# Kernel optimization log

Hardware: AMD Instinct MI355X
Metric: run time of the kernel (lower is better)

The kernel has to match this reference:

```python
import jax, jax.numpy as jnp
import numpy as np

HEADS = 8
DIM_HEAD = 64
DIM = 256
INNER = HEADS * DIM_HEAD  # 512


def setup_inputs() -> dict:
    key = jax.random.key(0)
    ks = jax.random.split(key, 5)
    b_times_r, n = 32, 1024
    x = jax.random.normal(ks[0], (b_times_r, n, DIM), dtype=jnp.float32)
    # nn.Linear weights stored as (in, out) so y = x @ W
    Wq = jax.random.normal(ks[1], (DIM, INNER), dtype=jnp.float32) * 0.02
    Wkv = jax.random.normal(ks[2], (DIM, 2 * INNER), dtype=jnp.float32) * 0.02
    Wout = jax.random.normal(ks[3], (INNER, DIM), dtype=jnp.float32) * 0.02
    bout = jax.random.normal(ks[4], (DIM,), dtype=jnp.float32) * 0.02
    return {"x": x, "Wq": Wq, "Wkv": Wkv, "Wout": Wout, "bout": bout, "tie_attn_dim": 32}


def reference(x, Wq, Wkv, Wout, bout, tie_attn_dim):
    r = tie_attn_dim
    br, n, _ = x.shape
    b = br // r
    q = x @ Wq                                   # (b*r, n, inner)
    k, v = jnp.split(x @ Wkv, 2, axis=-1)        # (b*r, n, inner) each

    def split_heads(t):
        # (b*r) n (h d) -> b r h n d
        return t.reshape(b, r, n, HEADS, DIM_HEAD).transpose(0, 1, 3, 2, 4)

    q, k, v = map(split_heads, (q, k, v))
    scale = (DIM_HEAD ** -0.5) * (r ** -0.5)
    # tied attention: sum logits over the MSA row dim r
    dots = jnp.einsum('brhid,brhjd->bhij', q, k) * scale  # (b, h, n, n)
    attn = jax.nn.softmax(dots, axis=-1)
    out = jnp.einsum('bhij,brhjd->brhid', attn, v)        # (b, r, h, n, d)
    out = out.transpose(0, 1, 3, 2, 4).reshape(br, n, INNER)
    return out @ Wout + bout
```

## Files before the change

kernel.cpp:

```cpp
#include <hip/hip_runtime.h>
#include <math.h>

typedef unsigned short bf16u;
typedef __attribute__((ext_vector_type(8))) short short8;
typedef __attribute__((ext_vector_type(4))) float f32x4;

__device__ __forceinline__ bf16u f2bf(float f) {
    unsigned int u = __float_as_uint(f);
    u += 0x7fffu + ((u >> 16) & 1u);
    return (bf16u)(u >> 16);
}
__device__ __forceinline__ float bf2f(bf16u h) {
    return __uint_as_float(((unsigned int)h) << 16);
}

__device__ __forceinline__ void gload16(const void* g, void* s) {
    __builtin_amdgcn_global_load_lds((const __attribute__((address_space(1))) void*)g,
                                     (__attribute__((address_space(3))) void*)s, 16, 0, 0);
}

#define MM(a_, b_, c_) c_ = __builtin_amdgcn_mfma_f32_16x16x32_bf16(a_, b_, c_, 0, 0, 0)
#define BAR() __builtin_amdgcn_s_barrier()

#define STG() do { if (q < nht) { \
    const int t_ = q >> 2, p_ = q & 3; \
    const bf16u* P_ = (p_ < 2) ? B : A; \
    const long s_ = ((p_ < 2) ? brow : arow) + ((p_ & 1) ? r128 : 0) + t_ * 64; \
    bf16u* d_ = S + ((t_ & 1) << 15) + ((p_ < 2) ? 16384 : 0) + ((p_ & 1) << 12) + (w << 9); \
    gload16(P_ + s_, d_); \
    gload16(P_ + s_ + 32, d_ + 8192); \
  } ++q; } while (0)

#define RDA(dst, t, m, kk) dst = *(const short8*)(S + (((t) & 1) << 15) + ((kk) << 13) + ((wr * 8 + (m)) << 9) + (l << 3))
#define RDB(dst, t, n, kk) dst = *(const short8*)(S + (((t) & 1) << 15) + 16384 + ((kk) << 13) + ((wc * 4 + (n)) << 9) + (l << 3))

#define KTILE(t, VMASM) do { \
   \
  RDA(af[0][0],t,0,0); RDA(af[0][1],t,0,1); RDA(af[1][0],t,1,0); RDA(af[1][1],t,1,1); \
  RDA(af[2][0],t,2,0); RDA(af[2][1],t,2,1); RDA(af[3][0],t,3,0); RDA(af[3][1],t,3,1); \
  RDB(b0[0][0],t,0,0); RDB(b0[0][1],t,0,1); RDB(b0[1][0],t,1,0); RDB(b0[1][1],t,1,1); \
  STG(); \
  BAR(); \
  __builtin_amdgcn_s_setprio(1); \
  MM(af[0][0],b0[0][0],acc[0][0]); MM(af[0][1],b0[0][1],acc[0][0]); \
  MM(af[0][0],b0[1][0],acc[0][1]); MM(af[0][1],b0[1][1],acc[0][1]); \
  MM(af[1][0],b0[0][0],acc[1][0]); MM(af[1][1],b0[0][1],acc[1][0]); \
  MM(af[1][0],b0[1][0],acc[1][1]); MM(af[1][1],b0[1][1],acc[1][1]); \
  MM(af[2][0],b0[0][0],acc[2][0]); MM(af[2][1],b0[0][1],acc[2][0]); \
  MM(af[2][0],b0[1][0],acc[2][1]); MM(af[2][1],b0[1][1],acc[2][1]); \
  MM(af[3][0],b0[0][0],acc[3][0]); MM(af[3][1],b0[0][1],acc[3][0]); \
  MM(af[3][0],b0[1][0],acc[3][1]); MM(af[3][1],b0[1][1],acc[3][1]); \
  __builtin_amdgcn_s_setprio(0); \
  BAR(); \
   \
  RDB(b1[0][0],t,2,0); RDB(b1[0][1],t,2,1); RDB(b1[1][0],t,3,0); RDB(b1[1][1],t,3,1); \
  STG(); \
  BAR(); \
  __builtin_amdgcn_s_setprio(1); \
  MM(af[0][0],b1[0][0],acc[0][2]); MM(af[0][1],b1[0][1],acc[0][2]); \
  MM(af[0][0],b1[1][0],acc[0][3]); MM(af[0][1],b1[1][1],acc[0][3]); \
  MM(af[1][0],b1[0][0],acc[1][2]); MM(af[1][1],b1[0][1],acc[1][2]); \
  MM(af[1][0],b1[1][0],acc[1][3]); MM(af[1][1],b1[1][1],acc[1][3]); \
  MM(af[2][0],b1[0][0],acc[2][2]); MM(af[2][1],b1[0][1],acc[2][2]); \
  MM(af[2][0],b1[1][0],acc[2][3]); MM(af[2][1],b1[1][1],acc[2][3]); \
  MM(af[3][0],b1[0][0],acc[3][2]); MM(af[3][1],b1[0][1],acc[3][2]); \
  MM(af[3][0],b1[1][0],acc[3][3]); MM(af[3][1],b1[1][1],acc[3][3]); \
  __builtin_amdgcn_s_setprio(0); \
  BAR(); \
   \
  RDA(af[0][0],t,4,0); RDA(af[0][1],t,4,1); RDA(af[1][0],t,5,0); RDA(af[1][1],t,5,1); \
  RDA(af[2][0],t,6,0); RDA(af[2][1],t,6,1); RDA(af[3][0],t,7,0); RDA(af[3][1],t,7,1); \
  STG(); \
  BAR(); \
  __builtin_amdgcn_s_setprio(1); \
  MM(af[0][0],b1[0][0],acc[4][2]); MM(af[0][1],b1[0][1],acc[4][2]); \
  MM(af[0][0],b1[1][0],acc[4][3]); MM(af[0][1],b1[1][1],acc[4][3]); \
  MM(af[1][0],b1[0][0],acc[5][2]); MM(af[1][1],b1[0][1],acc[5][2]); \
  MM(af[1][0],b1[1][0],acc[5][3]); MM(af[1][1],b1[1][1],acc[5][3]); \
  MM(af[2][0],b1[0][0],acc[6][2]); MM(af[2][1],b1[0][1],acc[6][2]); \
  MM(af[2][0],b1[1][0],acc[6][3]); MM(af[2][1],b1[1][1],acc[6][3]); \
  MM(af[3][0],b1[0][0],acc[7][2]); MM(af[3][1],b1[0][1],acc[7][2]); \
  MM(af[3][0],b1[1][0],acc[7][3]); MM(af[3][1],b1[1][1],acc[7][3]); \
  __builtin_amdgcn_s_setprio(0); \
  BAR(); \
   \
  STG(); \
  BAR(); \
  __builtin_amdgcn_s_setprio(1); \
  MM(af[0][0],b0[0][0],acc[4][0]); MM(af[0][1],b0[0][1],acc[4][0]); \
  MM(af[0][0],b0[1][0],acc[4][1]); MM(af[0][1],b0[1][1],acc[4][1]); \
  MM(af[1][0],b0[0][0],acc[5][0]); MM(af[1][1],b0[0][1],acc[5][0]); \
  MM(af[1][0],b0[1][0],acc[5][1]); MM(af[1][1],b0[1][1],acc[5][1]); \
  MM(af[2][0],b0[0][0],acc[6][0]); MM(af[2][1],b0[0][1],acc[6][0]); \
  MM(af[2][0],b0[1][0],acc[6][1]); MM(af[2][1],b0[1][1],acc[6][1]); \
  MM(af[3][0],b0[0][0],acc[7][0]); MM(af[3][1],b0[0][1],acc[7][0]); \
  MM(af[3][0],b0[1][0],acc[7][1]); MM(af[3][1],b0[1][1],acc[7][1]); \
  __builtin_amdgcn_s_setprio(0); \
  VMASM; \
  BAR(); \
} while (0)

template<int EPI>
__global__ __launch_bounds__(512, 2) void gemm8(
    const bf16u* __restrict__ Aall, const bf16u* __restrict__ Ball, int K,
    long sAz, long sBz,
    bf16u* __restrict__ D0, bf16u* __restrict__ D1, bf16u* __restrict__ D2,
    float* __restrict__ Df, const float* __restrict__ bias, float scale)
{
    const int gx = gridDim.x, gy = gridDim.y;
    const int nwg = gx * gy * gridDim.z;
    int flat = blockIdx.x + gx * (blockIdx.y + gy * blockIdx.z);
    int swz = (nwg & 7) ? flat : (flat & 7) * (nwg >> 3) + (flat >> 3);
    const int bx = swz % gx;
    int tq = swz / gx;
    const int by = tq % gy;
    const int z = tq / gy;

    const int tid = threadIdx.x;
    const int l = tid & 63, w = tid >> 6;
    const int fr = l & 15, fq = l >> 4;
    const int wr = w >> 2, wc = w & 3;
    const bf16u* A = Aall + (long)z * sAz;
    const bf16u* B = Ball + (long)z * sBz;
    const int m0 = by << 8, n0 = bx << 8;

    __shared__ __align__(16) bf16u S[65536];

    f32x4 acc[8][4];
#pragma unroll
    for (int i = 0; i < 8; ++i)
#pragma unroll
        for (int j = 0; j < 4; ++j) acc[i][j] = (f32x4){0.f, 0.f, 0.f, 0.f};

    const int NT = K >> 6;
    const int nht = NT << 2;
    const int NI = NT >> 1;
    int q = 0;

    const long arow = (long)(m0 + w * 16 + fr) * K + fq * 8;
    const long brow = (long)(n0 + w * 16 + fr) * K + fq * 8;
    const long r128 = (long)128 * K;

    STG(); STG(); STG(); STG(); STG(); STG();
    asm volatile("s_waitcnt vmcnt(4)" ::: "memory");
    BAR();

    short8 af[4][2], b0[2][2], b1[2][2];

    for (int i = 0; i < NI - 1; ++i) {
        KTILE(2 * i,     asm volatile("s_waitcnt vmcnt(4)" ::: "memory"));
        KTILE(2 * i + 1, asm volatile("s_waitcnt vmcnt(4)" ::: "memory"));
    }
    KTILE(2 * NI - 2, asm volatile("s_waitcnt vmcnt(0)" ::: "memory"));
    KTILE(2 * NI - 1, (void)0);

    const int colb = n0 + wc * 64;
    const int rowb = m0 + wr * 128;
    if constexpr (EPI == 1) {
        if (n0 >= 1024) {
            __syncthreads();
#pragma unroll
            for (int m = 0; m < 8; ++m)
#pragma unroll
                for (int n = 0; n < 4; ++n) {
                    const int cl = wc * 64 + n * 16 + fr;
                    const int rl = wr * 128 + m * 16 + fq * 4;
                    ushort4 pk;
                    pk.x = f2bf(acc[m][n][0]); pk.y = f2bf(acc[m][n][1]);
                    pk.z = f2bf(acc[m][n][2]); pk.w = f2bf(acc[m][n][3]);
                    *(ushort4*)(S + cl * 256 + rl) = pk;
                }
            __syncthreads();
            const int c2 = n0 - 1024;
            const int rr = m0 >> 10, i0 = m0 & 1023;
            const int rowt = tid >> 5;
            const int c0 = (tid & 31) * 8;
#pragma unroll
            for (int p = 0; p < 16; ++p) {
                const int row = p * 16 + rowt;
                const int hd = c2 + row;
                const int h = hd >> 6, d = hd & 63;
                *(short8*)(D2 + (((long)(h * 2048 + rr * 64 + d)) << 10) + i0 + c0)
                    = *(const short8*)(S + row * 256 + c0);
            }
        } else {
#pragma unroll
            for (int m = 0; m < 8; ++m)
#pragma unroll
                for (int n = 0; n < 4; ++n) {
                    const int col = colb + n * 16 + fr;
                    const int rb = rowb + m * 16 + fq * 4;
#pragma unroll
                    for (int r = 0; r < 4; ++r) {
                        const int row = rb + r;
                        const int rr = row >> 10, i = row & 1023;
                        const float val = acc[m][n][r];
                        if (col < 512) {
                            const int h = col >> 6, d = col & 63;
                            D0[((long)(h * 1024 + i) << 11) + rr * 64 + d] = f2bf(val);
                        } else {
                            const int c = col - 512, h = c >> 6, d = c & 63;
                            D1[((long)(h * 1024 + i) << 11) + rr * 64 + d] = f2bf(val);
                        }
                    }
                }
        }
    } else if constexpr (EPI == 2) {
#pragma unroll
        for (int m = 0; m < 8; ++m)
#pragma unroll
            for (int n = 0; n < 4; ++n) {
                const int col = colb + n * 16 + fr;
                const int rb = rowb + m * 16 + fq * 4;
#pragma unroll
                for (int r = 0; r < 4; ++r)
                    D0[((long)z << 20) + ((long)(rb + r) << 10) + col] = f2bf(acc[m][n][r] * scale);
            }
    } else if constexpr (EPI == 3) {
#pragma unroll
        for (int m = 0; m < 8; ++m)
#pragma unroll
            for (int n = 0; n < 4; ++n) {
                const int col = colb + n * 16 + fr;
                const int cb = col >> 6, d = col & 63;
                const int rb = rowb + m * 16 + fq * 4;
#pragma unroll
                for (int r = 0; r < 4; ++r)
                    D0[((long)(cb * 1024 + rb + r) << 9) + z * 64 + d] = f2bf(acc[m][n][r]);
            }
    } else {
#pragma unroll
        for (int m = 0; m < 8; ++m)
#pragma unroll
            for (int n = 0; n < 4; ++n) {
                const int col = colb + n * 16 + fr;
                const int rb = rowb + m * 16 + fq * 4;
#pragma unroll
                for (int r = 0; r < 4; ++r)
                    Df[(long)(rb + r) * 256 + col] = acc[m][n][r] + bias[col];
            }
    }
}

__global__ __launch_bounds__(256) void cvt_x(const float* __restrict__ in,
                                             bf16u* __restrict__ out) {
    const long idx = (long)(blockIdx.x * 256 + threadIdx.x) * 4;
    const float4 v = *(const float4*)(in + idx);
    ushort4 o;
    o.x = f2bf(v.x); o.y = f2bf(v.y); o.z = f2bf(v.z); o.w = f2bf(v.w);
    *(ushort4*)(out + idx) = o;
}

__global__ __launch_bounds__(256) void transpose_cvt(const float* __restrict__ in,
                                                     bf16u* __restrict__ out,
                                                     int R, int C) {
    const int idx = blockIdx.x * 256 + threadIdx.x;
    if (idx < R * C) {
        const int r = idx / C, c = idx % C;
        out[(long)c * R + r] = f2bf(in[idx]);
    }
}

__global__ __launch_bounds__(256) void softmax_rows(bf16u* __restrict__ att) {
    const long base = (long)blockIdx.x << 10;
    const int tid = threadIdx.x;
    const uint2 u = *(const uint2*)(att + base + tid * 4);
    const float v0 = bf2f(u.x & 0xffffu), v1 = bf2f(u.x >> 16);
    const float v2 = bf2f(u.y & 0xffffu), v3 = bf2f(u.y >> 16);
    float m = fmaxf(fmaxf(v0, v1), fmaxf(v2, v3));
#pragma unroll
    for (int o = 32; o; o >>= 1) m = fmaxf(m, __shfl_xor(m, o));
    __shared__ float red[8];
    if ((tid & 63) == 0) red[tid >> 6] = m;
    __syncthreads();
    m = fmaxf(fmaxf(red[0], red[1]), fmaxf(red[2], red[3]));
    const float e0 = __expf(v0 - m), e1 = __expf(v1 - m);
    const float e2 = __expf(v2 - m), e3 = __expf(v3 - m);
    float s = e0 + e1 + e2 + e3;
#pragma unroll
    for (int o = 32; o; o >>= 1) s += __shfl_xor(s, o);
    if ((tid & 63) == 0) red[4 + (tid >> 6)] = s;
    __syncthreads();
    const float inv = 1.0f / (red[4] + red[5] + red[6] + red[7]);
    uint2 o2;
    o2.x = (unsigned)f2bf(e0 * inv) | ((unsigned)f2bf(e1 * inv) << 16);
    o2.y = (unsigned)f2bf(e2 * inv) | ((unsigned)f2bf(e3 * inv) << 16);
    *(uint2*)(att + base + tid * 4) = o2;
}

extern "C" void kernel_launch(void* const* d_in, const int* in_sizes, int n_in,
                              void* d_out, int out_size, void* d_ws, size_t ws_size,
                              hipStream_t stream) {
    (void)in_sizes; (void)n_in; (void)out_size; (void)ws_size;
    const float* x    = (const float*)d_in[0];
    const float* Wq   = (const float*)d_in[1];
    const float* Wkv  = (const float*)d_in[2];
    const float* Wout = (const float*)d_in[3];
    const float* bout = (const float*)d_in[4];
    float* out = (float*)d_out;

    char* ws = (char*)d_ws;
    bf16u* xb    = (bf16u*)(ws);
    bf16u* WqkvT = (bf16u*)(ws + 16777216);
    bf16u* WoutT = (bf16u*)(ws + 17563648);
    bf16u* Qt    = (bf16u*)(ws + 17825792);
    bf16u* Kt    = (bf16u*)(ws + 51380224);
    bf16u* Vt2   = (bf16u*)(ws + 84934656);
    bf16u* att   = (bf16u*)(ws + 118489088);
    bf16u* out2  = (bf16u*)(ws + 135266304);

    cvt_x<<<8192, 256, 0, stream>>>(x, xb);
    transpose_cvt<<<512, 256, 0, stream>>>(Wq, WqkvT, 256, 512);
    transpose_cvt<<<1024, 256, 0, stream>>>(Wkv, WqkvT + 512 * 256, 256, 1024);
    transpose_cvt<<<512, 256, 0, stream>>>(Wout, WoutT, 512, 256);

    const float scale = 1.0f / (8.0f * sqrtf(32.0f));

    gemm8<1><<<dim3(6, 128, 1), 512, 0, stream>>>(
        xb, WqkvT, 256, 0, 0, Qt, Kt, Vt2, nullptr, nullptr, 0.f);

    gemm8<2><<<dim3(4, 4, 8), 512, 0, stream>>>(
        Qt, Kt, 2048, 1024L * 2048, 1024L * 2048, att, nullptr, nullptr, nullptr, nullptr, scale);

    softmax_rows<<<8192, 256, 0, stream>>>(att);

    gemm8<3><<<dim3(8, 4, 8), 512, 0, stream>>>(
        att, Vt2, 1024, 1024L * 1024, 2048L * 1024, out2, nullptr, nullptr, nullptr, nullptr, 0.f);

    gemm8<4><<<dim3(1, 128, 1), 512, 0, stream>>>(
        out2, WoutT, 512, 0, 0, nullptr, nullptr, nullptr, out, bout, 0.f);
}
```

Baseline: 289.2 us.

## Split-K the QK^T GEMM and use smaller-tile GEMM for projections

```diff
diff --git a/kernel.cpp b/kernel.cpp
--- a/kernel.cpp
+++ b/kernel.cpp
@@ -17,6 +17,147 @@
 __device__ __forceinline__ void gload16(const void* g, void* s) {
     __builtin_amdgcn_global_load_lds((const __attribute__((address_space(1))) void*)g,
                                      (__attribute__((address_space(3))) void*)s, 16, 0, 0);
+}
+
+template<int EPI>
+__global__ __launch_bounds__(256, 4) void gemm_bt(
+    const bf16u* __restrict__ Aall, const bf16u* __restrict__ Ball, int K,
+    long strideAz, long strideBz,
+    bf16u* __restrict__ D0, bf16u* __restrict__ D1, bf16u* __restrict__ D2,
+    float* __restrict__ Df, const float* __restrict__ bias, float scale)
+{
+    const int gx = gridDim.x, gy = gridDim.y;
+    const int nwg = gx * gy * gridDim.z;
+    int flat = blockIdx.x + gx * (blockIdx.y + gy * blockIdx.z);
+    int swz = (nwg & 7) ? flat : (flat & 7) * (nwg >> 3) + (flat >> 3);
+    const int bx = swz % gx;
+    const int t1 = swz / gx;
+    const int by = t1 % gy;
+    const int z  = t1 / gy;
+
+    const int tid = threadIdx.x;
+    const int l = tid & 63, w = tid >> 6;
+    const int fr = l & 15, fq = l >> 4;
+    const int kb = fq * 8;
+    const bf16u* A = Aall + (long)z * strideAz;
+    const bf16u* B = Ball + (long)z * strideBz;
+    const int m0 = by * 128, n0 = bx * 128;
+
+    __shared__ __align__(16) bf16u S[16384];
+
+    f32x4 acc[4][4];
+#pragma unroll
+    for (int i = 0; i < 4; ++i)
+#pragma unroll
+        for (int j = 0; j < 4; ++j) acc[i][j] = (f32x4){0.f, 0.f, 0.f, 0.f};
+
+    const long aoff0 = (long)(m0 + w * 16 + fr) * K + kb;
+    const long aoff1 = (long)(m0 + (w + 4) * 16 + fr) * K + kb;
+    const long boff0 = (long)(n0 + w * 16 + fr) * K + kb;
+    const long boff1 = (long)(n0 + (w + 4) * 16 + fr) * K + kb;
+
+    const int wr = w >> 1, wc = w & 1;
+
+#define STAGE(c, k0) do { \
+        bf16u* as_ = S + (c) * 4096; \
+        bf16u* bs_ = S + 8192 + (c) * 4096; \
+        gload16(A + aoff0 + (k0), as_ + w * 512); \
+        gload16(A + aoff1 + (k0), as_ + w * 512 + 2048); \
+        gload16(B + boff0 + (k0), bs_ + w * 512); \
+        gload16(B + boff1 + (k0), bs_ + w * 512 + 2048); \
+    } while (0)
+
+    STAGE(0, 0);
+    __syncthreads();
+
+    int cur = 0;
+    for (int k0 = 0; k0 < K; k0 += 32) {
+        if (k0 + 32 < K) STAGE(cur ^ 1, k0 + 32);
+
+        const bf16u* Ac = S + cur * 4096;
+        const bf16u* Bc = S + 8192 + cur * 4096;
+        short8 af[4], bg[4];
+#pragma unroll
+        for (int t = 0; t < 4; ++t) {
+            af[t] = *(const short8*)(Ac + (wr * 4 + t) * 512 + l * 8);
+            bg[t] = *(const short8*)(Bc + (wc * 4 + t) * 512 + l * 8);
+        }
+#pragma unroll
+        for (int mt = 0; mt < 4; ++mt)
+#pragma unroll
+            for (int nt = 0; nt < 4; ++nt)
+                acc[mt][nt] = __builtin_amdgcn_mfma_f32_16x16x32_bf16(
+                    af[mt], bg[nt], acc[mt][nt], 0, 0, 0);
+        __syncthreads();
+        cur ^= 1;
+    }
+#undef STAGE
+
+    if constexpr (EPI == 1) {
+        if (n0 >= 1024) {
+#pragma unroll
+            for (int mt = 0; mt < 4; ++mt) {
+#pragma unroll
+                for (int nt = 0; nt < 4; ++nt) {
+                    const f32x4 v = acc[mt][nt];
+                    const int cl = wc * 64 + nt * 16 + fr;
+                    const int rl = wr * 64 + mt * 16 + fq * 4;
+                    ushort4 pk;
+                    pk.x = f2bf(v[0]); pk.y = f2bf(v[1]);
+                    pk.z = f2bf(v[2]); pk.w = f2bf(v[3]);
+                    *(ushort4*)(S + cl * 128 + rl) = pk;
+                }
+            }
+            __syncthreads();
+            const int c2 = n0 - 1024;
+            const int rr = m0 >> 10, i0 = m0 & 1023;
+            const int rowt = tid >> 4, c0 = (tid & 15) * 8;
+#pragma unroll
+            for (int p = 0; p < 8; ++p) {
+                const int row = p * 16 + rowt;
+                const int col = c2 + row;
+                const int h = col >> 6, d = col & 63;
+                const short8 vv = *(const short8*)(S + row * 128 + c0);
+                *(short8*)(D2 + ((long)(h * 2048 + rr * 64 + d) << 10) + i0 + c0) = vv;
+            }
+        } else {
+#pragma unroll
+            for (int mt = 0; mt < 4; ++mt) {
+#pragma unroll
+                for (int nt = 0; nt < 4; ++nt) {
+                    const f32x4 v = acc[mt][nt];
+                    const int col = n0 + wc * 64 + nt * 16 + fr;
+                    const int rbase = m0 + wr * 64 + mt * 16 + fq * 4;
+#pragma unroll
+                    for (int r = 0; r < 4; ++r) {
+                        const float val = v[r];
+                        const int row = rbase + r;
+                        const int rr = row >> 10, i = row & 1023;
+                        if (col < 512) {
+                            const int h = col >> 6, d = col & 63;
+                            D0[((long)(h * 1024 + i) << 11) + rr * 64 + d] = f2bf(val);
+                        } else {
+                            const int c = col - 512, h = c >> 6, d = c & 63;
+                            D1[((long)(h * 1024 + i) << 11) + rr * 64 + d] = f2bf(val);
+                        }
+                    }
+                }
+            }
+        }
+    } else {
+#pragma unroll
+        for (int mt = 0; mt < 4; ++mt) {
+#pragma unroll
+            for (int nt = 0; nt < 4; ++nt) {
+                const f32x4 v = acc[mt][nt];
+                const int col = n0 + wc * 64 + nt * 16 + fr;
+                const int rbase = m0 + wr * 64 + mt * 16 + fq * 4;
+#pragma unroll
+                for (int r = 0; r < 4; ++r)
+                    Df[(long)(rbase + r) * 256 + col] = v[r] + bias[col];
+            }
+        }
+    }
 }
 
 #define MM(a_, b_, c_) c_ = __builtin_amdgcn_mfma_f32_16x16x32_bf16(a_, b_, c_, 0, 0, 0)
@@ -35,7 +176,6 @@
 #define RDB(dst, t, n, kk) dst = *(const short8*)(S + (((t) & 1) << 15) + 16384 + ((kk) << 13) + ((wc * 4 + (n)) << 9) + (l << 3))
 
 #define KTILE(t, VMASM) do { \
-   \
   RDA(af[0][0],t,0,0); RDA(af[0][1],t,0,1); RDA(af[1][0],t,1,0); RDA(af[1][1],t,1,1); \
   RDA(af[2][0],t,2,0); RDA(af[2][1],t,2,1); RDA(af[3][0],t,3,0); RDA(af[3][1],t,3,1); \
   RDB(b0[0][0],t,0,0); RDB(b0[0][1],t,0,1); RDB(b0[1][0],t,1,0); RDB(b0[1][1],t,1,1); \
@@ -52,7 +192,6 @@
   MM(af[3][0],b0[1][0],acc[3][1]); MM(af[3][1],b0[1][1],acc[3][1]); \
   __builtin_amdgcn_s_setprio(0); \
   BAR(); \
-   \
   RDB(b1[0][0],t,2,0); RDB(b1[0][1],t,2,1); RDB(b1[1][0],t,3,0); RDB(b1[1][1],t,3,1); \
   STG(); \
   BAR(); \
@@ -67,7 +206,6 @@
   MM(af[3][0],b1[1][0],acc[3][3]); MM(af[3][1],b1[1][1],acc[3][3]); \
   __builtin_amdgcn_s_setprio(0); \
   BAR(); \
-   \
   RDA(af[0][0],t,4,0); RDA(af[0][1],t,4,1); RDA(af[1][0],t,5,0); RDA(af[1][1],t,5,1); \
   RDA(af[2][0],t,6,0); RDA(af[2][1],t,6,1); RDA(af[3][0],t,7,0); RDA(af[3][1],t,7,1); \
   STG(); \
@@ -83,7 +221,6 @@
   MM(af[3][0],b1[1][0],acc[7][3]); MM(af[3][1],b1[1][1],acc[7][3]); \
   __builtin_amdgcn_s_setprio(0); \
   BAR(); \
-   \
   STG(); \
   BAR(); \
   __builtin_amdgcn_s_setprio(1); \
@@ -102,10 +239,9 @@
 
 template<int EPI>
 __global__ __launch_bounds__(512, 2) void gemm8(
-    const bf16u* __restrict__ Aall, const bf16u* __restrict__ Ball, int K,
-    long sAz, long sBz,
-    bf16u* __restrict__ D0, bf16u* __restrict__ D1, bf16u* __restrict__ D2,
-    float* __restrict__ Df, const float* __restrict__ bias, float scale)
+    const bf16u* __restrict__ Aall, const bf16u* __restrict__ Ball,
+    int Kld, int Kloop, long splitOff, long sAz, long sBz,
+    bf16u* __restrict__ D0, float scale)
 {
     const int gx = gridDim.x, gy = gridDim.y;
     const int nwg = gx * gy * gridDim.z;
@@ -120,8 +256,8 @@
     const int l = tid & 63, w = tid >> 6;
     const int fr = l & 15, fq = l >> 4;
     const int wr = w >> 2, wc = w & 3;
-    const bf16u* A = Aall + (long)z * sAz;
-    const bf16u* B = Ball + (long)z * sBz;
+    const bf16u* A = Aall + (long)(z & 7) * sAz + (long)(z >> 3) * splitOff;
+    const bf16u* B = Ball + (long)(z & 7) * sBz + (long)(z >> 3) * splitOff;
     const int m0 = by << 8, n0 = bx << 8;
 
     __shared__ __align__(16) bf16u S[65536];
@@ -132,14 +268,14 @@
 #pragma unroll
         for (int j = 0; j < 4; ++j) acc[i][j] = (f32x4){0.f, 0.f, 0.f, 0.f};
 
-    const int NT = K >> 6;
+    const int NT = Kloop >> 6;
     const int nht = NT << 2;
     const int NI = NT >> 1;
     int q = 0;
 
-    const long arow = (long)(m0 + w * 16 + fr) * K + fq * 8;
-    const long brow = (long)(n0 + w * 16 + fr) * K + fq * 8;
-    const long r128 = (long)128 * K;
+    const long arow = (long)(m0 + w * 16 + fr) * Kld + fq * 8;
+    const long brow = (long)(n0 + w * 16 + fr) * Kld + fq * 8;
+    const long r128 = (long)128 * Kld;
 
     STG(); STG(); STG(); STG(); STG(); STG();
     asm volatile("s_waitcnt vmcnt(4)" ::: "memory");
@@ -156,56 +292,7 @@
 
     const int colb = n0 + wc * 64;
     const int rowb = m0 + wr * 128;
-    if constexpr (EPI == 1) {
-        if (n0 >= 1024) {
-            __syncthreads();
-#pragma unroll
-            for (int m = 0; m < 8; ++m)
-#pragma unroll
-                for (int n = 0; n < 4; ++n) {
-                    const int cl = wc * 64 + n * 16 + fr;
-                    const int rl = wr * 128 + m * 16 + fq * 4;
-                    ushort4 pk;
-                    pk.x = f2bf(acc[m][n][0]); pk.y = f2bf(acc[m][n][1]);
-                    pk.z = f2bf(acc[m][n][2]); pk.w = f2bf(acc[m][n][3]);
-                    *(ushort4*)(S + cl * 256 + rl) = pk;
-                }
-            __syncthreads();
-            const int c2 = n0 - 1024;
-            const int rr = m0 >> 10, i0 = m0 & 1023;
-            const int rowt = tid >> 5;
-            const int c0 = (tid & 31) * 8;
-#pragma unroll
-            for (int p = 0; p < 16; ++p) {
-                const int row = p * 16 + rowt;
-                const int hd = c2 + row;
-                const int h = hd >> 6, d = hd & 63;
-                *(short8*)(D2 + (((long)(h * 2048 + rr * 64 + d)) << 10) + i0 + c0)
-                    = *(const short8*)(S + row * 256 + c0);
-            }
-        } else {
-#pragma unroll
-            for (int m = 0; m < 8; ++m)
-#pragma unroll
-                for (int n = 0; n < 4; ++n) {
-                    const int col = colb + n * 16 + fr;
-                    const int rb = rowb + m * 16 + fq * 4;
-#pragma unroll
-                    for (int r = 0; r < 4; ++r) {
-                        const int row = rb + r;
-                        const int rr = row >> 10, i = row & 1023;
-                        const float val = acc[m][n][r];
-                        if (col < 512) {
-                            const int h = col >> 6, d = col & 63;
-                            D0[((long)(h * 1024 + i) << 11) + rr * 64 + d] = f2bf(val);
-                        } else {
-                            const int c = col - 512, h = c >> 6, d = c & 63;
-                            D1[((long)(h * 1024 + i) << 11) + rr * 64 + d] = f2bf(val);
-                        }
-                    }
-                }
-        }
-    } else if constexpr (EPI == 2) {
+    if constexpr (EPI == 2) {
 #pragma unroll
         for (int m = 0; m < 8; ++m)
 #pragma unroll
@@ -216,7 +303,7 @@
                 for (int r = 0; r < 4; ++r)
                     D0[((long)z << 20) + ((long)(rb + r) << 10) + col] = f2bf(acc[m][n][r] * scale);
             }
-    } else if constexpr (EPI == 3) {
+    } else {
 #pragma unroll
         for (int m = 0; m < 8; ++m)
 #pragma unroll
@@ -226,18 +313,7 @@
                 const int rb = rowb + m * 16 + fq * 4;
 #pragma unroll
                 for (int r = 0; r < 4; ++r)
-                    D0[((long)(cb * 1024 + rb + r) << 9) + z * 64 + d] = f2bf(acc[m][n][r]);
-            }
-    } else {
-#pragma unroll
-        for (int m = 0; m < 8; ++m)
-#pragma unroll
-            for (int n = 0; n < 4; ++n) {
-                const int col = colb + n * 16 + fr;
-                const int rb = rowb + m * 16 + fq * 4;
-#pragma unroll
-                for (int r = 0; r < 4; ++r)
-                    Df[(long)(rb + r) * 256 + col] = acc[m][n][r] + bias[col];
+                    D0[((long)(cb * 1024 + rb + r) << 9) + (z & 7) * 64 + d] = f2bf(acc[m][n][r]);
             }
     }
 }
@@ -261,12 +337,16 @@
     }
 }
 
-__global__ __launch_bounds__(256) void softmax_rows(bf16u* __restrict__ att) {
+__global__ __launch_bounds__(256) void softmax_rows2(const bf16u* __restrict__ attP,
+                                                     bf16u* __restrict__ att) {
     const long base = (long)blockIdx.x << 10;
     const int tid = threadIdx.x;
-    const uint2 u = *(const uint2*)(att + base + tid * 4);
-    const float v0 = bf2f(u.x & 0xffffu), v1 = bf2f(u.x >> 16);
-    const float v2 = bf2f(u.y & 0xffffu), v3 = bf2f(u.y >> 16);
+    const uint2 u0 = *(const uint2*)(attP + base + tid * 4);
+    const uint2 u1 = *(const uint2*)(attP + 8388608 + base + tid * 4);
+    const float v0 = bf2f(u0.x & 0xffffu) + bf2f(u1.x & 0xffffu);
+    const float v1 = bf2f(u0.x >> 16)     + bf2f(u1.x >> 16);
+    const float v2 = bf2f(u0.y & 0xffffu) + bf2f(u1.y & 0xffffu);
+    const float v3 = bf2f(u0.y >> 16)     + bf2f(u1.y >> 16);
     float m = fmaxf(fmaxf(v0, v1), fmaxf(v2, v3));
 #pragma unroll
     for (int o = 32; o; o >>= 1) m = fmaxf(m, __shfl_xor(m, o));
@@ -308,6 +388,7 @@
     bf16u* Vt2   = (bf16u*)(ws + 84934656);
     bf16u* att   = (bf16u*)(ws + 118489088);
     bf16u* out2  = (bf16u*)(ws + 135266304);
+    bf16u* attP  = out2;
 
     cvt_x<<<8192, 256, 0, stream>>>(x, xb);
     transpose_cvt<<<512, 256, 0, stream>>>(Wq, WqkvT, 256, 512);
@@ -316,17 +397,17 @@
 
     const float scale = 1.0f / (8.0f * sqrtf(32.0f));
 
-    gemm8<1><<<dim3(6, 128, 1), 512, 0, stream>>>(
+    gemm_bt<1><<<dim3(12, 256, 1), 256, 0, stream>>>(
         xb, WqkvT, 256, 0, 0, Qt, Kt, Vt2, nullptr, nullptr, 0.f);
 
-    gemm8<2><<<dim3(4, 4, 8), 512, 0, stream>>>(
-        Qt, Kt, 2048, 1024L * 2048, 1024L * 2048, att, nullptr, nullptr, nullptr, nullptr, scale);
-
-    softmax_rows<<<8192, 256, 0, stream>>>(att);
+    gemm8<2><<<dim3(4, 4, 16), 512, 0, stream>>>(
+        Qt, Kt, 2048, 1024, 1024, 1024L * 2048, 1024L * 2048, attP, scale);
+
+    softmax_rows2<<<8192, 256, 0, stream>>>(attP, att);
 
     gemm8<3><<<dim3(8, 4, 8), 512, 0, stream>>>(
-        att, Vt2, 1024, 1024L * 1024, 2048L * 1024, out2, nullptr, nullptr, nullptr, nullptr, 0.f);
-
-    gemm8<4><<<dim3(1, 128, 1), 512, 0, stream>>>(
+        att, Vt2, 1024, 1024, 0, 1024L * 1024, 2048L * 1024, out2, 0.f);
+
+    gemm_bt<4><<<dim3(2, 256, 1), 256, 0, stream>>>(
         out2, WoutT, 512, 0, 0, nullptr, nullptr, nullptr, out, bout, 0.f);
 }
```

Result: faster. 267.9 us (-7.4%).
